# Kernel optimization log

Measured on AMD Instinct MI355X. Metric: run time of the kernel, lower is better.

## Reference

```python
import jax, jax.numpy as jnp
import numpy as np

N_NODES = 50000

def mpnn_layer(x, edge_index, edge_weight, Wm, Wu, bu):
    # x: [N, Din]; Wm, Wu: [Dout, Din]; bu: [Dout]
    src, dst = edge_index[0], edge_index[1]
    m = x @ Wm.T                                   # [N, Dout] linear message
    msg = edge_weight[:, None] * m[src]            # gather + weight  [E, Dout]
    agg = jax.ops.segment_sum(msg, dst, num_segments=N_NODES)  # scatter-add
    return jnp.tanh(x @ Wu.T + bu + agg)

def setup_inputs() -> dict:
    key = jax.random.key(0)
    ks = jax.random.split(key, 16)
    N, E, D_IN, H, OUT = N_NODES, 800000, 128, 128, 32
    inp = {
        'x': jax.random.normal(ks[0], (N, D_IN), dtype=jnp.float32),
        'edge_index': jax.random.randint(ks[1], (2, E), 0, N, dtype=jnp.int64),
        'edge_weight': jax.random.uniform(ks[2], (E,), dtype=jnp.float32),
    }
    scale = 0.05
    dims = [D_IN, H, H]  # per-layer input dims
    for l in range(3):
        inp[f'Wm{l}'] = jax.random.normal(ks[3 + 3 * l], (H, dims[l]), dtype=jnp.float32) * scale
        inp[f'Wu{l}'] = jax.random.normal(ks[4 + 3 * l], (H, dims[l]), dtype=jnp.float32) * scale
        inp[f'bu{l}'] = jnp.zeros((H,), dtype=jnp.float32)
    inp['Wout'] = jax.random.normal(ks[13], (OUT, H), dtype=jnp.float32) * scale
    inp['bout'] = jnp.zeros((OUT,), dtype=jnp.float32)
    return inp

def reference(x, edge_index, edge_weight, Wm0, Wu0, bu0, Wm1, Wu1, bu1, Wm2, Wu2, bu2, Wout, bout):
    h = x
    for Wm, Wu, bu in ((Wm0, Wu0, bu0), (Wm1, Wu1, bu1), (Wm2, Wu2, bu2)):
        h = mpnn_layer(h, edge_index, edge_weight, Wm, Wu, bu)
    return h @ Wout.T + bout
```

## Files before the change

### kernel.cpp

```cpp
#include <hip/hip_runtime.h>
#include <hip/hip_bf16.h>
#include <cstddef>


typedef __attribute__((ext_vector_type(8))) short short8;
typedef __attribute__((ext_vector_type(4))) float f32x4;
typedef unsigned short ushort_t;
typedef unsigned int uint_t;
typedef __attribute__((ext_vector_type(4))) uint_t u32x4;

#define BSH 8
#define BSZ 256
#define CAPB 6144
#define TSTRIDE 16
#define EPB 2048

__device__ inline ushort_t f2bf(float f) {
    uint_t u = __float_as_uint(f);
    uint_t r = u + 0x7FFFu + ((u >> 16) & 1u);
    return (ushort_t)(r >> 16);
}
__device__ inline float bf_lo(uint_t u) { return __uint_as_float(u << 16); }
__device__ inline float bf_hi(uint_t u) { return __uint_as_float(u & 0xFFFF0000u); }
__device__ inline uint_t packbf(float a, float b) {
    return (uint_t)f2bf(a) | ((uint_t)f2bf(b) << 16);
}

__device__ inline float fast_tanh(float x) {
    float e = __builtin_amdgcn_exp2f(x * 2.8853900817779268f);
    return 1.f - 2.f * __builtin_amdgcn_rcpf(e + 1.f);
}

__device__ inline int get_dst(const int* __restrict__ ei, int e, int E, int f) {
    if (f) return ei[E + e];
    return ((const int2*)ei)[(size_t)E + e].x;
}
__device__ inline int get_src(const int* __restrict__ ei, int e, int E, int f) {
    if (f) return ei[e];
    return ((const int2*)ei)[e].x;
}

struct SetupArgs {
    const float* Wm0; const float* Wu0;
    const float* Wm1; const float* Wu1;
    const float* Wm2; const float* Wu2;
    const float* Wout;
    const float* x; const int* ei;
    ushort_t* wswz;
    ushort_t* woswz;
    ushort_t* xb;
    int* tails;
    int* flag;
    int N, E, TI;
    int ZT, WB, XB;
};
__global__ __launch_bounds__(256) void setup_kernel(SetupArgs a) {
    int bx = blockIdx.x, t = threadIdx.x;
    if (bx < a.ZT) {
        int i = bx * 256 + t;
        if (i < a.TI) a.tails[i] = 0;
        return;
    }
    bx -= a.ZT;
    if (bx == 0) {
        __shared__ int any;
        if (t == 0) any = 0;
        __syncthreads();
        int n = a.E < 2048 ? a.E : 2048;
        for (int i = t; i < n; i += 256)
            if (a.ei[2 * i + 1] != 0) any = 1;
        __syncthreads();
        if (t == 0) a.flag[0] = any;
        return;
    }
    bx -= 1;
    if (bx < a.WB) {
        int i = bx * 256 + t;
        if (i < 3 * 32768) {
            int l = i >> 15, r2 = i & 32767;
            int ct = r2 >> 12, ks = (r2 >> 9) & 7, lane = (r2 >> 3) & 63, j = r2 & 7;
            int col = ct * 16 + (lane & 15);
            int k = ks * 32 + (lane >> 4) * 8 + j;
            const float* Wm = l == 0 ? a.Wm0 : (l == 1 ? a.Wm1 : a.Wm2);
            const float* Wu = l == 0 ? a.Wu0 : (l == 1 ? a.Wu1 : a.Wu2);
            float v = k < 128 ? Wm[col * 128 + k] : Wu[col * 128 + (k - 128)];
            a.wswz[(size_t)l * 32768 + r2] = f2bf(v);
        } else if (i < 3 * 32768 + 4096) {
            int r2 = i - 3 * 32768;
            int ct = r2 >> 11, ks = (r2 >> 9) & 3, lane = (r2 >> 3) & 63, j = r2 & 7;
            int col = ct * 16 + (lane & 15);
            int k = ks * 32 + (lane >> 4) * 8 + j;
            a.woswz[r2] = f2bf(a.Wout[col * 128 + k]);
        }
        return;
    }
    bx -= a.WB;
    {
        int j = bx * 256 + t;
        if (j < a.N * 32) {
            float4 v = *(const float4*)(a.x + (size_t)j * 4);
            uint2 o;
            o.x = packbf(v.x, v.y);
            o.y = packbf(v.z, v.w);
            *(uint2*)(a.xb + (size_t)j * 4) = o;
        }
    }
}

__global__ __launch_bounds__(256) void bin_kernel(
    const int* __restrict__ ei, const float* __restrict__ ew,
    const int* __restrict__ flag, int* __restrict__ tails,
    uint2* __restrict__ staged, int E, int NB) {
    __shared__ uint2 ent[EPB];
    __shared__ uint2 srt[EPB];
    __shared__ int cnt[256], cur[256], exc[256], runbase[256];
    const int tid = threadIdx.x;
    const int e0 = blockIdx.x * EPB;
    const int nE = (E - e0) < EPB ? (E - e0) : EPB;
    const int f = flag[0];
    cnt[tid] = 0;
    cur[tid] = 0;
    __syncthreads();
    for (int i = tid; i < nE; i += 256) {
        int e = e0 + i;
        int s = get_src(ei, e, E, f);
        int d = get_dst(ei, e, E, f);
        uint2 v;
        v.x = (uint_t)s | ((uint_t)f2bf(ew[e]) << 16);
        v.y = (uint_t)d;
        ent[i] = v;
        atomicAdd(&cnt[d >> BSH], 1);
    }
    __syncthreads();
    exc[tid] = cnt[tid];
    __syncthreads();
    for (int o = 1; o < 256; o <<= 1) {
        int v = tid >= o ? exc[tid - o] : 0;
        __syncthreads();
        exc[tid] += v;
        __syncthreads();
    }
    exc[tid] -= cnt[tid];
    if (tid < NB) {
        int c = cnt[tid];
        runbase[tid] = c ? atomicAdd(&tails[tid * TSTRIDE], c) : 0;
    }
    __syncthreads();
    for (int i = tid; i < nE; i += 256) {
        uint2 v = ent[i];
        int b = (int)(v.y >> BSH);
        int lp = atomicAdd(&cur[b], 1);
        srt[exc[b] + lp] = v;
    }
    __syncthreads();
    for (int i = tid; i < nE; i += 256) {
        uint2 v = srt[i];
        int b = (int)(v.y >> BSH);
        int gp = runbase[b] + (i - exc[b]);
        if (gp < CAPB) {
            uint2 o;
            o.x = v.x;
            o.y = (uint_t)(v.y & (BSZ - 1));
            staged[(size_t)b * CAPB + gp] = o;
        }
    }
}

__global__ __launch_bounds__(256) void place_kernel(
    const uint2* __restrict__ staged, const int* __restrict__ tails,
    int* __restrict__ cursor, uint_t* __restrict__ csr,
    int2* __restrict__ rowdeg, int N) {
    __shared__ int cnt[256], cur[256], excl[256], sm[256];
    __shared__ int baseSh;
    __shared__ uint_t outb[CAPB];
    const int b = blockIdx.x, tid = threadIdx.x;
    const int node0 = b << BSH;
    int tot = tails[b * TSTRIDE];
    tot = tot < CAPB ? tot : CAPB;
    cnt[tid] = 0;
    __syncthreads();
    const uint2* sp = staged + ((size_t)b * CAPB);
    for (int i = tid; i < tot; i += 256) atomicAdd(&cnt[sp[i].y], 1);
    __syncthreads();
    int c0 = cnt[tid];
    sm[tid] = c0;
    __syncthreads();
    for (int o = 1; o < 256; o <<= 1) {
        int v = tid >= o ? sm[tid - o] : 0;
        __syncthreads();
        sm[tid] += v;
        __syncthreads();
    }
    if (tid == 255) baseSh = atomicAdd(cursor, sm[255]);
    excl[tid] = sm[tid] - c0;
    cur[tid] = 0;
    __syncthreads();
    const int base = baseSh;
    for (int i = tid; i < tot; i += 256) {
        uint2 e = sp[i];
        int pos = excl[e.y] + atomicAdd(&cur[e.y], 1);
        outb[pos] = e.x;
    }
    __syncthreads();
    for (int i = tid; i < tot; i += 256) csr[base + i] = outb[i];
    if (node0 + tid < N) {
        int2 be;
        be.x = base + excl[tid];
        be.y = base + excl[tid] + c0;
        rowdeg[node0 + tid] = be;
    }
}

template <int WITH_OUT>
__global__ __launch_bounds__(256, 4) void fused_layer(
    const uint_t* __restrict__ csr, const int2* __restrict__ rowdeg,
    const ushort_t* __restrict__ h, const ushort_t* __restrict__ Wswz,
    const float* __restrict__ bias, ushort_t* __restrict__ Hout,
    const ushort_t* __restrict__ Woswz, const float* __restrict__ bout,
    float* __restrict__ Cout, int N) {
    __shared__ ushort_t Gt[16 * 128];
    __shared__ ushort_t Ht[16 * 128];
    const int tid = threadIdx.x;
    const int lane = tid & 63;
    const int wv = tid >> 6;
    const int R0 = blockIdx.x * 16;
    const int sl = lane >> 4, fl = lane & 15;

    const int pp = tid * 16;
    const int srow = pp >> 8;
    const int sx = (pp & 255) ^ ((srow & 7) << 4);
    uint4 hst = *(const uint4*)(h + (size_t)(R0 + srow) * 128 + (sx >> 1));

    int begs[4], degs[4];
    uint_t cent[4];
#pragma unroll
    for (int i = 0; i < 4; ++i) {
        int nd = R0 + wv * 4 + i;
        int bg = 0, dg = 0;
        if (nd < N) { int2 be = rowdeg[nd]; bg = be.x; dg = be.y - be.x; }
        begs[i] = bg; degs[i] = dg;
        cent[i] = 0;
        if (dg > 0) {
            int idx = lane & 31;
            idx = idx < dg ? idx : dg - 1;
            cent[i] = csr[bg + idx];
        }
    }

    float sacc[4][8];
#pragma unroll
    for (int i = 0; i < 4; ++i)
#pragma unroll
        for (int r = 0; r < 8; ++r) sacc[i][r] = 0.f;

#pragma unroll
    for (int i = 0; i < 4; ++i) {
        uint_t pw[8];
        const ushort_t* ra[8];
#pragma unroll
        for (int b = 0; b < 8; ++b) {
            uint_t p = __shfl(cent[i], (b * 4 + sl) & 31, 64);
            pw[b] = p;
            ra[b] = h + (size_t)(p & 0xFFFFu) * 128 + fl * 8;
        }
        u32x4 v[8];
        if (degs[i] > 16) {
#pragma unroll
            for (int b = 0; b < 8; ++b) v[b] = *(const u32x4*)ra[b];
            __builtin_amdgcn_sched_group_barrier(0x020, 8, 0);
#pragma unroll
            for (int b = 0; b < 8; ++b) {
                float w = ((b * 4 + sl) < degs[i]) ? bf_hi(pw[b]) : 0.f;
                sacc[i][0] += w * bf_lo(v[b][0]); sacc[i][1] += w * bf_hi(v[b][0]);
                sacc[i][2] += w * bf_lo(v[b][1]); sacc[i][3] += w * bf_hi(v[b][1]);
                sacc[i][4] += w * bf_lo(v[b][2]); sacc[i][5] += w * bf_hi(v[b][2]);
                sacc[i][6] += w * bf_lo(v[b][3]); sacc[i][7] += w * bf_hi(v[b][3]);
            }
        } else {
#pragma unroll
            for (int b = 0; b < 4; ++b) v[b] = *(const u32x4*)ra[b];
            __builtin_amdgcn_sched_group_barrier(0x020, 4, 0);
#pragma unroll
            for (int b = 0; b < 4; ++b) {
                float w = ((b * 4 + sl) < degs[i]) ? bf_hi(pw[b]) : 0.f;
                sacc[i][0] += w * bf_lo(v[b][0]); sacc[i][1] += w * bf_hi(v[b][0]);
                sacc[i][2] += w * bf_lo(v[b][1]); sacc[i][3] += w * bf_hi(v[b][1]);
                sacc[i][4] += w * bf_lo(v[b][2]); sacc[i][5] += w * bf_hi(v[b][2]);
                sacc[i][6] += w * bf_lo(v[b][3]); sacc[i][7] += w * bf_hi(v[b][3]);
            }
        }
        if (degs[i] > 32) {
            for (int j = begs[i] + 32 + sl; j < begs[i] + degs[i]; j += 4) {
                uint_t p = csr[j];
                float w = bf_hi(p);
                u32x4 vv = *(const u32x4*)(h + (size_t)(p & 0xFFFFu) * 128 + fl * 8);
                sacc[i][0] += w * bf_lo(vv[0]); sacc[i][1] += w * bf_hi(vv[0]);
                sacc[i][2] += w * bf_lo(vv[1]); sacc[i][3] += w * bf_hi(vv[1]);
                sacc[i][4] += w * bf_lo(vv[2]); sacc[i][5] += w * bf_hi(vv[2]);
                sacc[i][6] += w * bf_lo(vv[3]); sacc[i][7] += w * bf_hi(vv[3]);
            }
        }
    }

#pragma unroll
    for (int i = 0; i < 4; ++i) {
#pragma unroll
        for (int r = 0; r < 8; ++r) {
            sacc[i][r] += __shfl_xor(sacc[i][r], 16, 64);
            sacc[i][r] += __shfl_xor(sacc[i][r], 32, 64);
        }
        if (sl == 0) {
            uint4 o;
            o.x = packbf(sacc[i][0], sacc[i][1]);
            o.y = packbf(sacc[i][2], sacc[i][3]);
            o.z = packbf(sacc[i][4], sacc[i][5]);
            o.w = packbf(sacc[i][6], sacc[i][7]);
            const int lr = wv * 4 + i;
            *(uint4*)(Gt + lr * 128 + ((fl * 8) ^ ((lr & 7) << 3))) = o;
        }
    }
    *(uint4*)((char*)Ht + pp) = hst;
    __syncthreads();

    const int m = lane & 15, kg = lane >> 4;
    const int lsw = (m & 7) << 3;
    const int colL = lane & 15, rq = lane >> 4;

    short8 b0f[8], b1f[8];
#pragma unroll
    for (int ksp = 0; ksp < 8; ++ksp) {
        b0f[ksp] = *(const short8*)(Wswz + (((2 * wv) * 8 + ksp) * 64 + lane) * 8);
        b1f[ksp] = *(const short8*)(Wswz + (((2 * wv + 1) * 8 + ksp) * 64 + lane) * 8);
    }
    const float bv0 = bias[(2 * wv) * 16 + colL];
    const float bv1 = bias[(2 * wv + 1) * 16 + colL];

    f32x4 acc0 = (f32x4){0.f, 0.f, 0.f, 0.f};
    f32x4 acc1 = (f32x4){0.f, 0.f, 0.f, 0.f};
#pragma unroll
    for (int ksp = 0; ksp < 8; ++ksp) {
        const ushort_t* tp = (ksp < 4) ? Gt : Ht;
        short8 av = *(const short8*)(tp + m * 128 + (((ksp & 3) * 32 + kg * 8) ^ lsw));
        acc0 = __builtin_amdgcn_mfma_f32_16x16x32_bf16(av, b0f[ksp], acc0, 0, 0, 0);
        acc1 = __builtin_amdgcn_mfma_f32_16x16x32_bf16(av, b1f[ksp], acc1, 0, 0, 0);
    }
    float v0[4], v1[4];
#pragma unroll
    for (int reg = 0; reg < 4; ++reg) {
        v0[reg] = fast_tanh(acc0[reg] + bv0);
        v1[reg] = fast_tanh(acc1[reg] + bv1);
    }

    if (WITH_OUT == 0) {
#pragma unroll
        for (int reg = 0; reg < 4; ++reg) {
            int gr = R0 + rq * 4 + reg;
            if (gr < N) {
                Hout[(size_t)gr * 128 + (2 * wv) * 16 + colL] = f2bf(v0[reg]);
                Hout[(size_t)gr * 128 + (2 * wv + 1) * 16 + colL] = f2bf(v1[reg]);
            }
        }
    } else {
        __syncthreads();
#pragma unroll
        for (int reg = 0; reg < 4; ++reg) {
            int lr3 = rq * 4 + reg;
            int sw3 = (lr3 & 7) << 3;
            Gt[lr3 * 128 + (((2 * wv) * 16 + colL) ^ sw3)] = f2bf(v0[reg]);
            Gt[lr3 * 128 + (((2 * wv + 1) * 16 + colL) ^ sw3)] = f2bf(v1[reg]);
        }
        __syncthreads();
        if (wv < 2) {
            const int oc = wv;
            const int osw = (m & 7) << 3;
            short8 ob[4];
#pragma unroll
            for (int ks = 0; ks < 4; ++ks)
                ob[ks] = *(const short8*)(Woswz + ((oc * 4 + ks) * 64 + lane) * 8);
            f32x4 oacc = (f32x4){0.f, 0.f, 0.f, 0.f};
#pragma unroll
            for (int ks = 0; ks < 4; ++ks) {
                short8 av = *(const short8*)(Gt + m * 128 + ((ks * 32 + kg * 8) ^ osw));
                oacc = __builtin_amdgcn_mfma_f32_16x16x32_bf16(av, ob[ks], oacc, 0, 0, 0);
            }
            const float obv = bout[oc * 16 + colL];
#pragma unroll
            for (int reg = 0; reg < 4; ++reg) {
                int gr = R0 + rq * 4 + reg;
                if (gr < N) Cout[(size_t)gr * 32 + oc * 16 + colL] = oacc[reg] + obv;
            }
        }
    }
}

extern "C" void kernel_launch(void* const* d_in, const int* in_sizes, int n_in,
                              void* d_out, int out_size, void* d_ws, size_t ws_size,
                              hipStream_t stream) {
    const float* x   = (const float*)d_in[0];
    const int* ei    = (const int*)d_in[1];
    const float* ew  = (const float*)d_in[2];
    const float* Wm[3] = {(const float*)d_in[3], (const float*)d_in[6], (const float*)d_in[9]};
    const float* Wu[3] = {(const float*)d_in[4], (const float*)d_in[7], (const float*)d_in[10]};
    const float* bu[3] = {(const float*)d_in[5], (const float*)d_in[8], (const float*)d_in[11]};
    const float* Wout = (const float*)d_in[12];
    const float* bout = (const float*)d_in[13];
    float* out = (float*)d_out;

    const int N = in_sizes[0] / 128;
    const int E = in_sizes[2];
    const size_t NPAD = 50048;
    const int NB = (N + BSZ - 1) / BSZ;
    const int TI = NB * TSTRIDE + 16;

    ushort_t* xb    = (ushort_t*)d_ws;
    ushort_t* hA    = xb + NPAD * 128;
    ushort_t* hB    = hA + NPAD * 128;
    ushort_t* gbuf  = hB + NPAD * 128;
    ushort_t* wswz  = gbuf + NPAD * 128;
    ushort_t* woswz = wswz + 3 * 32768;
    int* flag       = (int*)(woswz + 4096);
    int* tails      = flag + 1;
    int* cursor     = tails + NB * TSTRIDE;
    int* endp       = tails + TI;
    int2* rowdeg    = (int2*)(((uintptr_t)endp + 7) & ~(uintptr_t)7);
    uint2* staged   = (uint2*)(rowdeg + N + 8);
    uint_t* csr     = (uint_t*)(staged + (size_t)NB * CAPB);
    (void)ws_size;

    const int ZT = (TI + 255) / 256;
    const int WB = (3 * 32768 + 4096 + 255) / 256;
    const int XB = (N * 32 + 255) / 256;
    const int gB = (E + EPB - 1) / EPB;
    const int gF = (N + 15) / 16;

    SetupArgs sa;
    sa.Wm0 = Wm[0]; sa.Wu0 = Wu[0];
    sa.Wm1 = Wm[1]; sa.Wu1 = Wu[1];
    sa.Wm2 = Wm[2]; sa.Wu2 = Wu[2];
    sa.Wout = Wout; sa.x = x; sa.ei = ei;
    sa.wswz = wswz; sa.woswz = woswz; sa.xb = xb;
    sa.tails = tails; sa.flag = flag;
    sa.N = N; sa.E = E; sa.TI = TI;
    sa.ZT = ZT; sa.WB = WB; sa.XB = XB;
    setup_kernel<<<ZT + 1 + WB + XB, 256, 0, stream>>>(sa);

    bin_kernel<<<gB, 256, 0, stream>>>(ei, ew, flag, tails, staged, E, NB);
    place_kernel<<<NB, 256, 0, stream>>>(staged, tails, cursor, csr, rowdeg, N);

    fused_layer<0><<<gF, 256, 0, stream>>>(csr, rowdeg, xb, wswz, bu[0], hA,
                                           nullptr, nullptr, nullptr, N);
    fused_layer<0><<<gF, 256, 0, stream>>>(csr, rowdeg, hA, wswz + 32768, bu[1], hB,
                                           nullptr, nullptr, nullptr, N);
    fused_layer<1><<<gF, 256, 0, stream>>>(csr, rowdeg, hB, wswz + 2 * 32768, bu[2],
                                           nullptr, woswz, bout, out, N);
}
```

Measured before the change: 248.0 us.

## Double-buffer neighbor gathers across rows and relax launch bounds

The per-row gather loop is restructured into a two-stage software pipeline. The loads for the next row are issued before the previous row's loaded features are accumulated, using two register buffers (A/B), which is meant to hide gather latency. Launch bounds drop from 4 to 2 blocks per SM so the compiler can use more registers for the doubled buffers. The cost is higher register pressure and possibly lower occupancy, which may reduce latency hiding across waves.

```diff
diff --git a/kernel.cpp b/kernel.cpp
--- a/kernel.cpp
+++ b/kernel.cpp
@@ -211,8 +211,59 @@
     }
 }
 
+#define ISSUE(I, PW, V)                                                       \
+    do {                                                                      \
+        _Pragma("unroll")                                                     \
+        for (int b = 0; b < 8; ++b)                                           \
+            PW[b] = __shfl(cent[I], (b * 4 + sl) & 31, 64);                   \
+        if (degs[I] > 16) {                                                   \
+            _Pragma("unroll")                                                 \
+            for (int b = 0; b < 8; ++b)                                       \
+                V[b] = *(const u32x4*)(h + (size_t)(PW[b] & 0xFFFFu) * 128 +  \
+                                       fl * 8);                               \
+            __builtin_amdgcn_sched_group_barrier(0x020, 8, 0);                \
+        } else {                                                              \
+            _Pragma("unroll")                                                 \
+            for (int b = 0; b < 4; ++b)                                       \
+                V[b] = *(const u32x4*)(h + (size_t)(PW[b] & 0xFFFFu) * 128 +  \
+                                       fl * 8);                               \
+            __builtin_amdgcn_sched_group_barrier(0x020, 4, 0);                \
+        }                                                                     \
+    } while (0)
+
+#define CONSB(I, PW, V, B)                                                    \
+    do {                                                                      \
+        float w_ = ((B * 4 + sl) < degs[I]) ? bf_hi(PW[B]) : 0.f;             \
+        sacc[I][0] += w_ * bf_lo(V[B][0]); sacc[I][1] += w_ * bf_hi(V[B][0]); \
+        sacc[I][2] += w_ * bf_lo(V[B][1]); sacc[I][3] += w_ * bf_hi(V[B][1]); \
+        sacc[I][4] += w_ * bf_lo(V[B][2]); sacc[I][5] += w_ * bf_hi(V[B][2]); \
+        sacc[I][6] += w_ * bf_lo(V[B][3]); sacc[I][7] += w_ * bf_hi(V[B][3]); \
+    } while (0)
+
+#define CONSUME(I, PW, V)                                                     \
+    do {                                                                      \
+        CONSB(I, PW, V, 0); CONSB(I, PW, V, 1);                               \
+        CONSB(I, PW, V, 2); CONSB(I, PW, V, 3);                               \
+        if (degs[I] > 16) {                                                   \
+            CONSB(I, PW, V, 4); CONSB(I, PW, V, 5);                           \
+            CONSB(I, PW, V, 6); CONSB(I, PW, V, 7);                           \
+        }                                                                     \
+        if (degs[I] > 32) {                                                   \
+            for (int j = begs[I] + 32 + sl; j < begs[I] + degs[I]; j += 4) {  \
+                uint_t p = csr[j];                                            \
+                float w = bf_hi(p);                                           \
+                u32x4 vv = *(const u32x4*)(h + (size_t)(p & 0xFFFFu) * 128 +  \
+                                           fl * 8);                           \
+                sacc[I][0] += w * bf_lo(vv[0]); sacc[I][1] += w * bf_hi(vv[0]);\
+                sacc[I][2] += w * bf_lo(vv[1]); sacc[I][3] += w * bf_hi(vv[1]);\
+                sacc[I][4] += w * bf_lo(vv[2]); sacc[I][5] += w * bf_hi(vv[2]);\
+                sacc[I][6] += w * bf_lo(vv[3]); sacc[I][7] += w * bf_hi(vv[3]);\
+            }                                                                 \
+        }                                                                     \
+    } while (0)
+
 template <int WITH_OUT>
-__global__ __launch_bounds__(256, 4) void fused_layer(
+__global__ __launch_bounds__(256, 2) void fused_layer(
     const uint_t* __restrict__ csr, const int2* __restrict__ rowdeg,
     const ushort_t* __restrict__ h, const ushort_t* __restrict__ Wswz,
     const float* __restrict__ bias, ushort_t* __restrict__ Hout,
@@ -253,53 +304,17 @@
 #pragma unroll
         for (int r = 0; r < 8; ++r) sacc[i][r] = 0.f;
 
-#pragma unroll
-    for (int i = 0; i < 4; ++i) {
-        uint_t pw[8];
-        const ushort_t* ra[8];
-#pragma unroll
-        for (int b = 0; b < 8; ++b) {
-            uint_t p = __shfl(cent[i], (b * 4 + sl) & 31, 64);
-            pw[b] = p;
-            ra[b] = h + (size_t)(p & 0xFFFFu) * 128 + fl * 8;
-        }
-        u32x4 v[8];
-        if (degs[i] > 16) {
-#pragma unroll
-            for (int b = 0; b < 8; ++b) v[b] = *(const u32x4*)ra[b];
-            __builtin_amdgcn_sched_group_barrier(0x020, 8, 0);
-#pragma unroll
-            for (int b = 0; b < 8; ++b) {
-                float w = ((b * 4 + sl) < degs[i]) ? bf_hi(pw[b]) : 0.f;
-                sacc[i][0] += w * bf_lo(v[b][0]); sacc[i][1] += w * bf_hi(v[b][0]);
-                sacc[i][2] += w * bf_lo(v[b][1]); sacc[i][3] += w * bf_hi(v[b][1]);
-                sacc[i][4] += w * bf_lo(v[b][2]); sacc[i][5] += w * bf_hi(v[b][2]);
-                sacc[i][6] += w * bf_lo(v[b][3]); sacc[i][7] += w * bf_hi(v[b][3]);
-            }
-        } else {
-#pragma unroll
-            for (int b = 0; b < 4; ++b) v[b] = *(const u32x4*)ra[b];
-            __builtin_amdgcn_sched_group_barrier(0x020, 4, 0);
-#pragma unroll
-            for (int b = 0; b < 4; ++b) {
-                float w = ((b * 4 + sl) < degs[i]) ? bf_hi(pw[b]) : 0.f;
-                sacc[i][0] += w * bf_lo(v[b][0]); sacc[i][1] += w * bf_hi(v[b][0]);
-                sacc[i][2] += w * bf_lo(v[b][1]); sacc[i][3] += w * bf_hi(v[b][1]);
-                sacc[i][4] += w * bf_lo(v[b][2]); sacc[i][5] += w * bf_hi(v[b][2]);
-                sacc[i][6] += w * bf_lo(v[b][3]); sacc[i][7] += w * bf_hi(v[b][3]);
-            }
-        }
-        if (degs[i] > 32) {
-            for (int j = begs[i] + 32 + sl; j < begs[i] + degs[i]; j += 4) {
-                uint_t p = csr[j];
-                float w = bf_hi(p);
-                u32x4 vv = *(const u32x4*)(h + (size_t)(p & 0xFFFFu) * 128 + fl * 8);
-                sacc[i][0] += w * bf_lo(vv[0]); sacc[i][1] += w * bf_hi(vv[0]);
-                sacc[i][2] += w * bf_lo(vv[1]); sacc[i][3] += w * bf_hi(vv[1]);
-                sacc[i][4] += w * bf_lo(vv[2]); sacc[i][5] += w * bf_hi(vv[2]);
-                sacc[i][6] += w * bf_lo(vv[3]); sacc[i][7] += w * bf_hi(vv[3]);
-            }
-        }
+    {
+        uint_t pwA[8], pwB[8];
+        u32x4 vA[8], vB[8];
+        ISSUE(0, pwA, vA);
+        ISSUE(1, pwB, vB);
+        CONSUME(0, pwA, vA);
+        ISSUE(2, pwA, vA);
+        CONSUME(1, pwB, vB);
+        ISSUE(3, pwB, vB);
+        CONSUME(2, pwA, vA);
+        CONSUME(3, pwB, vB);
     }
 
 #pragma unroll
```

Measured after the change: 264.8 us. 1.07x slower.
